# Performance work log

Hardware: AMD Instinct MI355X
Metric: run time of the kernel (lower is better)

The kernel has to match this reference:

```python
import jax, jax.numpy as jnp
import numpy as np
from math import factorial

RS1 = [(16, 0), (8, 1), (4, 2)]
RS2 = [(16, 0), (8, 1), (4, 2)]


def _su2_cg(j1, j2, j3, m1, m2, m3):
    # Clebsch-Gordan coefficient <j1 m1 j2 m2 | j3 m3> (integer j's)
    if m3 != m1 + m2:
        return 0.0
    f = factorial
    vmin = int(max(-j1 + j2 + m3, -j1 + m1, 0))
    vmax = int(min(j2 + j3 + m1, j3 - j1 + j2, j3 + m3))
    C = ((2.0 * j3 + 1.0) * f(j3 + j1 - j2) * f(j3 - j1 + j2) * f(j1 + j2 - j3)
         * f(j3 + m3) * f(j3 - m3)
         / (f(j1 + j2 + j3 + 1) * f(j1 - m1) * f(j1 + m1) * f(j2 - m2) * f(j2 + m2))) ** 0.5
    S = 0.0
    for v in range(vmin, vmax + 1):
        S += (-1.0) ** (v + j2 + m2) * f(j2 + j3 + m1 - v) * f(j1 - m1 + v) \
             / (f(v) * f(j3 - j1 + j2 - v) * f(j3 + m3 - v) * f(v + j1 - j2 - m3))
    return C * S


def _su2_tensor(j1, j2, j3):
    C = np.zeros((2 * j1 + 1, 2 * j2 + 1, 2 * j3 + 1))
    for m1 in range(-j1, j1 + 1):
        for m2 in range(-j2, j2 + 1):
            m3 = m1 + m2
            if abs(m3) <= j3:
                C[m1 + j1, m2 + j2, m3 + j3] = _su2_cg(j1, j2, j3, m1, m2, m3)
    return C


def _change_basis_real_to_complex(l):
    q = np.zeros((2 * l + 1, 2 * l + 1), dtype=np.complex128)
    for m in range(-l, 0):
        q[l + m, l + abs(m)] = 2 ** -0.5
        q[l + m, l - abs(m)] = -1j * 2 ** -0.5
    q[l, l] = 1.0
    for m in range(1, l + 1):
        q[l + m, l + abs(m)] = (-1) ** m * 2 ** -0.5
        q[l + m, l - abs(m)] = 1j * (-1) ** m * 2 ** -0.5
    return ((-1j) ** l) * q


def _real_cg(l1, l2, l3):
    # CG tensor in the real spherical-harmonic basis, shape (2l1+1, 2l2+1, 2l3+1)
    C = _su2_tensor(l1, l2, l3)
    Q1 = _change_basis_real_to_complex(l1)
    Q2 = _change_basis_real_to_complex(l2)
    Q3 = _change_basis_real_to_complex(l3)
    C = np.einsum('ij,kl,mn,ikn->jlm', Q1, Q2, np.conj(Q3.T), C)
    return np.real(C)


def build_mixing_matrix(Rs1, Rs2):
    dim_in1 = sum(mul * (2 * l + 1) for mul, l in Rs1)
    dim_in2 = sum(mul * (2 * l + 1) for mul, l in Rs2)
    K = sum(m1 * m2 * (2 * l + 1)
            for m1, l1 in Rs1 for m2, l2 in Rs2
            for l in range(abs(l1 - l2), l1 + l2 + 1))
    M = np.zeros((K, dim_in1, dim_in2), dtype=np.float32)
    k_off = 0
    i_off = 0
    for mul1, l1 in Rs1:
        d1 = 2 * l1 + 1
        j_off = 0
        for mul2, l2 in Rs2:
            d2 = 2 * l2 + 1
            for l in range(abs(l1 - l2), l1 + l2 + 1):
                dl = 2 * l + 1
                # 'component' normalization
                C = (_real_cg(l1, l2, l) * (dl ** 0.5)).astype(np.float32)
                Ck = np.transpose(C, (2, 0, 1))  # (dl, d1, d2)
                for u in range(mul1):
                    for v in range(mul2):
                        k0 = k_off + (u * mul2 + v) * dl
                        M[k0:k0 + dl,
                          i_off + u * d1:i_off + (u + 1) * d1,
                          j_off + v * d2:j_off + (v + 1) * d2] = Ck
                k_off += mul1 * mul2 * dl
            j_off += mul2 * d2
        i_off += mul1 * d1
    return M


def setup_inputs() -> dict:
    key = jax.random.key(0)
    k1, k2 = jax.random.split(key)
    Z = 4096
    f1 = jax.random.normal(k1, (Z, 60), dtype=jnp.float32)
    f2 = jax.random.normal(k2, (Z, 60), dtype=jnp.float32)
    mix = jnp.asarray(build_mixing_matrix(RS1, RS2))  # (3600, 60, 60)
    return {"features_1": f1, "features_2": f2, "mixing_matrix": mix}


def reference(features_1, features_2, mixing_matrix):
    # output[z, k] = sum_{i,j} C[k,i,j] * f1[z,i] * f2[z,j]
    Z = features_1.shape[0]
    K, I, J = mixing_matrix.shape
    outer = jnp.einsum('zi,zj->zij', features_1, features_2).reshape(Z, I * J)
    return outer @ mixing_matrix.reshape(K, I * J).T
```

## Files before the change

### kernel.cpp

```cpp
#include <hip/hip_runtime.h>


#define ZT    32
#define NF    60
#define KTOT  3600
#define BLOCK 256

struct Seg { short kstart, mul2, dl, d1, d2, ioff, joff; };

__constant__ Seg c_segs[20] = {
  {   0,16,1,1,1, 0, 0},
  { 256, 8,3,1,3, 0,16},
  { 640, 4,5,1,5, 0,40},
  { 960,16,3,3,1,16, 0},
  {1344, 8,1,3,3,16,16},
  {1408, 8,3,3,3,16,16},
  {1600, 8,5,3,3,16,16},
  {1920, 4,3,3,5,16,40},
  {2016, 4,5,3,5,16,40},
  {2176, 4,7,3,5,16,40},
  {2400,16,5,5,1,40, 0},
  {2720, 8,3,5,3,40,16},
  {2816, 8,5,5,3,40,16},
  {2976, 8,7,5,3,40,16},
  {3200, 4,1,5,5,40,40},
  {3216, 4,3,5,5,40,40},
  {3264, 4,5,5,5,40,40},
  {3344, 4,7,5,5,40,40},
  {3456, 4,9,5,5,40,40},
  {3600, 0,1,1,1, 0, 0}
};

template<int D1, int D2>
__device__ __forceinline__ void tp_body(const float* __restrict__ Crow,
    int i0, int j0,
    const float (&f1s)[ZT][NF], const float (&f2s)[ZT][NF],
    float* __restrict__ out, int k, int z0)
{
  float c[D1 * D2];
#pragma unroll
  for (int ii = 0; ii < D1; ++ii)
#pragma unroll
    for (int jj = 0; jj < D2; ++jj)
      c[ii * D2 + jj] = Crow[(i0 + ii) * NF + (j0 + jj)];

#pragma unroll 2
  for (int zz = 0; zz < ZT; ++zz) {
    float r1[D1], r2[D2];
#pragma unroll
    for (int ii = 0; ii < D1; ++ii) r1[ii] = f1s[zz][i0 + ii];
#pragma unroll
    for (int jj = 0; jj < D2; ++jj) r2[jj] = f2s[zz][j0 + jj];
    float acc = 0.f;
#pragma unroll
    for (int ii = 0; ii < D1; ++ii)
#pragma unroll
      for (int jj = 0; jj < D2; ++jj)
        acc = fmaf(c[ii * D2 + jj], r1[ii] * r2[jj], acc);
    out[(size_t)(z0 + zz) * KTOT + k] = acc;
  }
}

__global__ __launch_bounds__(BLOCK) void tp_kernel(
    const float* __restrict__ f1, const float* __restrict__ f2,
    const float* __restrict__ M, float* __restrict__ out)
{
  __shared__ float f1s[ZT][NF];
  __shared__ float f2s[ZT][NF];
  const int z0 = blockIdx.y * ZT;

  const float* f1p = f1 + (size_t)z0 * NF;
  const float* f2p = f2 + (size_t)z0 * NF;
  for (int idx = threadIdx.x; idx < ZT * NF; idx += BLOCK) {
    (&f1s[0][0])[idx] = f1p[idx];
    (&f2s[0][0])[idx] = f2p[idx];
  }
  __syncthreads();

  const int k = blockIdx.x * BLOCK + (int)threadIdx.x;
  if (k >= KTOT) return;

  int s = 0;
#pragma unroll 1
  while (k >= c_segs[s + 1].kstart) ++s;
  const Seg sg = c_segs[s];

  const int local = k - sg.kstart;
  const int uv = local / sg.dl;
  const int u  = uv / sg.mul2;
  const int v  = uv - u * sg.mul2;
  const int i0 = sg.ioff + u * sg.d1;
  const int j0 = sg.joff + v * sg.d2;
  const float* Crow = M + (size_t)k * (NF * NF);

  if (sg.d1 == 1) {
    if (sg.d2 == 1)      tp_body<1,1>(Crow, i0, j0, f1s, f2s, out, k, z0);
    else if (sg.d2 == 3) tp_body<1,3>(Crow, i0, j0, f1s, f2s, out, k, z0);
    else                 tp_body<1,5>(Crow, i0, j0, f1s, f2s, out, k, z0);
  } else if (sg.d1 == 3) {
    if (sg.d2 == 1)      tp_body<3,1>(Crow, i0, j0, f1s, f2s, out, k, z0);
    else if (sg.d2 == 3) tp_body<3,3>(Crow, i0, j0, f1s, f2s, out, k, z0);
    else                 tp_body<3,5>(Crow, i0, j0, f1s, f2s, out, k, z0);
  } else {
    if (sg.d2 == 1)      tp_body<5,1>(Crow, i0, j0, f1s, f2s, out, k, z0);
    else if (sg.d2 == 3) tp_body<5,3>(Crow, i0, j0, f1s, f2s, out, k, z0);
    else                 tp_body<5,5>(Crow, i0, j0, f1s, f2s, out, k, z0);
  }
}

extern "C" void kernel_launch(void* const* d_in, const int* in_sizes, int n_in,
                              void* d_out, int out_size, void* d_ws, size_t ws_size,
                              hipStream_t stream) {
  const float* f1 = (const float*)d_in[0];
  const float* f2 = (const float*)d_in[1];
  const float* M  = (const float*)d_in[2];
  float* out = (float*)d_out;

  const int Z = in_sizes[0] / NF;
  dim3 grid((KTOT + BLOCK - 1) / BLOCK,
            Z / ZT);
  tp_kernel<<<grid, dim3(BLOCK), 0, stream>>>(f1, f2, M, out);
}
```

Before: 30.52 us.

## Transpose shared feature tiles to feature-major and vectorize z loads

Stores the f1/f2 shared tiles transposed as [feature][z] with padding, so each thread reads four consecutive z values with one 128-bit LDS load instead of scalar loads. The compute is refactored to factor the bilinear form (inner sum over the larger dimension, then a multiply by the other), which cuts FMAs per output. Global loads during staging become float4. The transposed staging writes are scattered scalar LDS stores, which may cause bank conflicts. The z loop is no longer unrolled.

```diff
diff --git a/kernel.cpp b/kernel.cpp
--- a/kernel.cpp
+++ b/kernel.cpp
@@ -2,9 +2,12 @@
 
 
 #define ZT    32
+#define ZPAD  36
 #define NF    60
 #define KTOT  3600
 #define BLOCK 256
+
+typedef float f32x4 __attribute__((ext_vector_type(4)));
 
 struct Seg { short kstart, mul2, dl, d1, d2, ioff, joff; };
 
@@ -34,7 +37,7 @@
 template<int D1, int D2>
 __device__ __forceinline__ void tp_body(const float* __restrict__ Crow,
     int i0, int j0,
-    const float (&f1s)[ZT][NF], const float (&f2s)[ZT][NF],
+    const float (&f1s)[NF][ZPAD], const float (&f2s)[NF][ZPAD],
     float* __restrict__ out, int k, int z0)
 {
   float c[D1 * D2];
@@ -44,20 +47,43 @@
     for (int jj = 0; jj < D2; ++jj)
       c[ii * D2 + jj] = Crow[(i0 + ii) * NF + (j0 + jj)];
 
-#pragma unroll 2
-  for (int zz = 0; zz < ZT; ++zz) {
-    float r1[D1], r2[D2];
-#pragma unroll
-    for (int ii = 0; ii < D1; ++ii) r1[ii] = f1s[zz][i0 + ii];
-#pragma unroll
-    for (int jj = 0; jj < D2; ++jj) r2[jj] = f2s[zz][j0 + jj];
-    float acc = 0.f;
+  float* op = out + (size_t)z0 * KTOT + k;
+
+#pragma unroll 1
+  for (int zz = 0; zz < ZT; zz += 4) {
+    f32x4 a[D1], b[D2];
 #pragma unroll
     for (int ii = 0; ii < D1; ++ii)
+      a[ii] = *(const f32x4*)&f1s[i0 + ii][zz];
 #pragma unroll
-      for (int jj = 0; jj < D2; ++jj)
-        acc = fmaf(c[ii * D2 + jj], r1[ii] * r2[jj], acc);
-    out[(size_t)(z0 + zz) * KTOT + k] = acc;
+    for (int jj = 0; jj < D2; ++jj)
+      b[jj] = *(const f32x4*)&f2s[j0 + jj][zz];
+
+    float* opz = op + (size_t)zz * KTOT;
+#pragma unroll
+    for (int q = 0; q < 4; ++q) {
+      float acc = 0.f;
+      if constexpr (D1 <= D2) {
+#pragma unroll
+        for (int ii = 0; ii < D1; ++ii) {
+          float t = 0.f;
+#pragma unroll
+          for (int jj = 0; jj < D2; ++jj)
+            t = fmaf(c[ii * D2 + jj], b[jj][q], t);
+          acc = fmaf(t, a[ii][q], acc);
+        }
+      } else {
+#pragma unroll
+        for (int jj = 0; jj < D2; ++jj) {
+          float t = 0.f;
+#pragma unroll
+          for (int ii = 0; ii < D1; ++ii)
+            t = fmaf(c[ii * D2 + jj], a[ii][q], t);
+          acc = fmaf(t, b[jj][q], acc);
+        }
+      }
+      opz[(size_t)q * KTOT] = acc;
+    }
   }
 }
 
@@ -65,15 +91,27 @@
     const float* __restrict__ f1, const float* __restrict__ f2,
     const float* __restrict__ M, float* __restrict__ out)
 {
-  __shared__ float f1s[ZT][NF];
-  __shared__ float f2s[ZT][NF];
+  __shared__ __align__(16) float f1s[NF][ZPAD];
+  __shared__ __align__(16) float f2s[NF][ZPAD];
   const int z0 = blockIdx.y * ZT;
 
-  const float* f1p = f1 + (size_t)z0 * NF;
-  const float* f2p = f2 + (size_t)z0 * NF;
-  for (int idx = threadIdx.x; idx < ZT * NF; idx += BLOCK) {
-    (&f1s[0][0])[idx] = f1p[idx];
-    (&f2s[0][0])[idx] = f2p[idx];
+  {
+    const float* f1p = f1 + (size_t)z0 * NF;
+    const float* f2p = f2 + (size_t)z0 * NF;
+    for (int t = threadIdx.x; t < (ZT * NF) / 4; t += BLOCK) {
+      f32x4 v = *(const f32x4*)(f1p + t * 4);
+      int zz = (t * 4) / NF;
+      int f0 = (t * 4) % NF;
+      f1s[f0 + 0][zz] = v[0]; f1s[f0 + 1][zz] = v[1];
+      f1s[f0 + 2][zz] = v[2]; f1s[f0 + 3][zz] = v[3];
+    }
+    for (int t = threadIdx.x; t < (ZT * NF) / 4; t += BLOCK) {
+      f32x4 v = *(const f32x4*)(f2p + t * 4);
+      int zz = (t * 4) / NF;
+      int f0 = (t * 4) % NF;
+      f2s[f0 + 0][zz] = v[0]; f2s[f0 + 1][zz] = v[1];
+      f2s[f0 + 2][zz] = v[2]; f2s[f0 + 3][zz] = v[3];
+    }
   }
   __syncthreads();
 
```

Measured after the change: 27.58 us. -9.6%, faster.
